# Kernel tuning notes

Measured on AMD Instinct MI355X. Metric: run time of the kernel, lower is better.

Reference implementation:

```python
import jax, jax.numpy as jnp
import numpy as np

TOPK = 2000        # post-score-sort candidates fed to NMS
NMS_THR = 0.5      # IOU suppression threshold


def get_iou(boxes1, boxes2):
    # boxes1: (A,4), boxes2: (B,4) in x1,y1,x2,y2 -> (A,B) IOU matrix
    area1 = (boxes1[:, 2] - boxes1[:, 0]) * (boxes1[:, 3] - boxes1[:, 1])
    area2 = (boxes2[:, 2] - boxes2[:, 0]) * (boxes2[:, 3] - boxes2[:, 1])
    lt = jnp.maximum(boxes1[:, None, :2], boxes2[None, :, :2])
    rb = jnp.minimum(boxes1[:, None, 2:], boxes2[None, :, 2:])
    wh = jnp.clip(rb - lt, 0.0)
    inter = wh[..., 0] * wh[..., 1]
    return inter / (area1[:, None] + area2[None, :] - inter)


def decode_boxes(box_transform_pred, boxes):
    # box_transform_pred: (N,C,4) dx,dy,dw,dh ; boxes: (N,4) -> (N,C,4)
    w = boxes[:, 2] - boxes[:, 0]
    h = boxes[:, 3] - boxes[:, 1]
    cx = boxes[:, 0] + 0.5 * w
    cy = boxes[:, 1] + 0.5 * h
    dx, dy, dw, dh = (box_transform_pred[..., i] for i in range(4))
    pcx = dx * w[:, None] + cx[:, None]
    pcy = dy * h[:, None] + cy[:, None]
    pw = jnp.exp(dw) * w[:, None]
    ph = jnp.exp(dh) * h[:, None]
    return jnp.stack((pcx - 0.5 * pw, pcy - 0.5 * ph,
                      pcx + 0.5 * pw, pcy + 0.5 * ph), axis=2)


def encode_boxes(gt, boxes):
    # boxes_to_transformation_targets: (N,4),(N,4) -> (N,4) tx,ty,tw,th
    w = boxes[:, 2] - boxes[:, 0]
    h = boxes[:, 3] - boxes[:, 1]
    cx = boxes[:, 0] + 0.5 * w
    cy = boxes[:, 1] + 0.5 * h
    gw = gt[:, 2] - gt[:, 0]
    gh = gt[:, 3] - gt[:, 1]
    gcx = gt[:, 0] + 0.5 * gw
    gcy = gt[:, 1] + 0.5 * gh
    return jnp.stack(((gcx - cx) / w, (gcy - cy) / h,
                      jnp.log(gw / w), jnp.log(gh / h)), axis=1)


def clamp_boxes(boxes, h, w):
    x1 = jnp.clip(boxes[..., 0], 0.0, w)
    y1 = jnp.clip(boxes[..., 1], 0.0, h)
    x2 = jnp.clip(boxes[..., 2], 0.0, w)
    y2 = jnp.clip(boxes[..., 3], 0.0, h)
    return jnp.stack((x1, y1, x2, y2), axis=-1)


def nms_keep(iou_kk, thr):
    # greedy NMS over score-sorted boxes; sequential via lax.scan
    K = iou_kk.shape[0]
    idx = jnp.arange(K)
    def step(suppressed, i):
        keep_i = ~suppressed[i]
        suppressed = suppressed | (keep_i & (iou_kk[i] > thr) & (idx > i))
        return suppressed, keep_i
    _, keep = jax.lax.scan(step, jnp.zeros((K,), bool), idx)
    return keep


def _make_boxes(key, n, h, w):
    k1, k2, k3, k4 = jax.random.split(key, 4)
    x1 = jax.random.uniform(k1, (n,)) * (w - 128.0)
    y1 = jax.random.uniform(k2, (n,)) * (h - 128.0)
    bw = jax.random.uniform(k3, (n,)) * 120.0 + 4.0
    bh = jax.random.uniform(k4, (n,)) * 120.0 + 4.0
    return jnp.stack((x1, y1, x1 + bw, y1 + bh), axis=1)


def setup_inputs() -> dict:
    key = jax.random.key(0)
    N, C, G, H, W = 200000, 21, 128, 800, 1333
    k1, k2, k3, k4 = jax.random.split(key, 4)
    return {
        "proposals": _make_boxes(k1, N, H, W),
        "box_transform_pred": jax.random.normal(k2, (N, C, 4)) * 0.1,
        "cls_scores": jax.random.normal(k3, (N, C)),
        "gt_boxes": _make_boxes(k4, G, H, W),
        "image_h": H,
        "image_w": W,
    }


def reference(proposals, box_transform_pred, cls_scores, gt_boxes, image_h, image_w):
    h = float(image_h); w = float(image_w)
    N = proposals.shape[0]
    # 1. decode all per-class boxes and clamp to image boundary  (N,C,4)
    pred_boxes = clamp_boxes(decode_boxes(box_transform_pred, proposals), h, w)
    iou = get_iou(gt_boxes, proposals)          # (G,N)
    best_idx = jnp.argmax(iou, axis=0)          # (N,)
    matched_gt = gt_boxes[best_idx]             # (N,4)
    reg_targets = encode_boxes(matched_gt, proposals)  # (N,4)
    # 3. per-proposal best foreground class score/box
    probs = jax.nn.softmax(cls_scores, axis=-1)
    fg = probs[:, 1:]
    score = jnp.max(fg, axis=-1)                # (N,)
    cls = jnp.argmax(fg, axis=-1) + 1           # (N,)
    idx = jnp.broadcast_to(cls[:, None, None], (N, 1, 4))
    box_per = jnp.take_along_axis(pred_boxes, idx, axis=1)[:, 0]  # (N,4)
    # 4. top-K by score, greedy NMS
    top_scores, top_idx = jax.lax.top_k(score, TOPK)
    top_boxes = box_per[top_idx]                # (K,4)
    keep = nms_keep(get_iou(top_boxes, top_boxes), NMS_THR)
    final = top_boxes * keep[:, None].astype(top_boxes.dtype)  # suppressed zeroed
    return jnp.concatenate([final, reg_targets], axis=0)
```

## Files before the change

kernel.cpp:

```cpp
#include <hip/hip_runtime.h>
#include <cstdint>

#define TOPK 2000
#define NMS_THR 0.5f
#define NCLS 21
#define HSHIFT 14
#define HBINS (1u << 16)
#define NCHUNK 256
#define CAND_CAP 4096
#define TPAD 2048

typedef unsigned long long u64;
typedef unsigned int u32;
typedef float f32x4 __attribute__((ext_vector_type(4)));

__device__ __forceinline__ u32 hperm(u32 bin) { return ((bin & 255u) << 8) | (bin >> 8); }

__device__ __forceinline__ float iou_pair(float ax1, float ay1, float ax2, float ay2, float aarea,
                                          float bx1, float by1, float bx2, float by2, float barea) {
#pragma clang fp contract(off)
    float ltx = fmaxf(ax1, bx1), lty = fmaxf(ay1, by1);
    float rbx = fminf(ax2, bx2), rby = fminf(ay2, by2);
    float wx = fmaxf(rbx - ltx, 0.f), wy = fmaxf(rby - lty, 0.f);
    float inter = wx * wy;
    return inter / (aarea + barea - inter);
}

__global__ __launch_bounds__(256) void k_prep(const float* __restrict__ cls,
                                              float* __restrict__ clsT,
                                              u32* __restrict__ hist, u32* __restrict__ csum,
                                              u32* __restrict__ meta, u32* __restrict__ rank,
                                              int N) {
    __shared__ float slds[256 * NCLS];
    int b = blockIdx.x, t = threadIdx.x;

    for (int v = b * 256 + t; v < (int)(HBINS / 4); v += gridDim.x * 256)
        ((uint4*)hist)[v] = make_uint4(0u, 0u, 0u, 0u);
    if (b == 0) {
        csum[t] = 0u;
        if (t < 64) meta[t] = 0u;
    }
    if (b < 16) rank[b * 256 + t] = 0u;

    int row0 = b * 256;
    int rows = N - row0;
    if (rows <= 0) return;
    if (rows > 256) rows = 256;
    if (rows == 256) {
        const uint4* __restrict__ src = (const uint4*)(cls + (size_t)row0 * NCLS);
        uint4* __restrict__ dst = (uint4*)slds;
        for (int v = t; v < 1344; v += 256) dst[v] = src[v];
    } else {
        int nw = rows * NCLS;
        const float* __restrict__ src = cls + (size_t)row0 * NCLS;
        for (int v = t; v < nw; v += 256) slds[v] = src[v];
    }
    __syncthreads();
    if (t < rows) {
#pragma unroll
        for (int c = 0; c < NCLS; ++c)
            clsT[(size_t)c * N + row0 + t] = slds[t * NCLS + c];
    }
}

__global__ __launch_bounds__(256, 3) void k_main(
    const float* __restrict__ prop, const float* __restrict__ btp,
    const float* __restrict__ clsT, const float* __restrict__ gt,
    const int* __restrict__ hptr, const int* __restrict__ wptr,
    float* __restrict__ out, float4* __restrict__ box_per,
    u32* __restrict__ score_bits, u32* __restrict__ hist,
    int N, int G) {
#pragma clang fp contract(off)
    __shared__ float4 sgt[256];
    __shared__ float sga[256];
    int tid = threadIdx.x;
    for (int g = tid; g < G; g += 256) {
        float4 gb = ((const float4*)gt)[g];
        sgt[g] = gb;
        sga[g] = (gb.z - gb.x) * (gb.w - gb.y);
    }
    __syncthreads();

    int i = blockIdx.x * 256 + tid;
    if (i >= N) return;

    float W = (float)wptr[0], H = (float)hptr[0];
    float4 p = ((const float4*)prop)[i];
    float pw = p.z - p.x, ph = p.w - p.y;
    float pcx = p.x + 0.5f * pw, pcy = p.y + 0.5f * ph;

    float e[NCLS];
#pragma unroll
    for (int c = 0; c < NCLS; ++c) e[c] = clsT[(size_t)c * N + i];

    float m = e[0];
#pragma unroll
    for (int c = 1; c < NCLS; ++c) m = fmaxf(m, e[c]);
#pragma unroll
    for (int c = 0; c < NCLS; ++c) e[c] = expf(e[c] - m);
    float Z = 0.f;
#pragma unroll
    for (int c = 0; c < NCLS; ++c) Z += e[c];
    float best = -1.f;
    int bc = 1;
#pragma unroll
    for (int c = 1; c < NCLS; ++c) {
        float pr = e[c] / Z;
        if (pr > best) { best = pr; bc = c; }
    }

    float4 t = ((const float4*)btp)[(size_t)i * NCLS + bc];

    u32 b = __float_as_uint(best);
    score_bits[i] = b;
    atomicAdd(&hist[hperm(b >> HSHIFT)], 1u);

    float parea = pw * ph;
    float bestiou = -1.f;
    int bi = 0;
    int g = 0;
    for (; g + 8 <= G; g += 8) {
        float4 g0 = sgt[g], g1 = sgt[g + 1], g2 = sgt[g + 2], g3 = sgt[g + 3];
        float4 g4 = sgt[g + 4], g5 = sgt[g + 5], g6 = sgt[g + 6], g7 = sgt[g + 7];
        float a0 = sga[g], a1 = sga[g + 1], a2 = sga[g + 2], a3 = sga[g + 3];
        float a4 = sga[g + 4], a5 = sga[g + 5], a6 = sga[g + 6], a7 = sga[g + 7];
        float v0 = iou_pair(g0.x, g0.y, g0.z, g0.w, a0, p.x, p.y, p.z, p.w, parea);
        float v1 = iou_pair(g1.x, g1.y, g1.z, g1.w, a1, p.x, p.y, p.z, p.w, parea);
        float v2 = iou_pair(g2.x, g2.y, g2.z, g2.w, a2, p.x, p.y, p.z, p.w, parea);
        float v3 = iou_pair(g3.x, g3.y, g3.z, g3.w, a3, p.x, p.y, p.z, p.w, parea);
        float v4 = iou_pair(g4.x, g4.y, g4.z, g4.w, a4, p.x, p.y, p.z, p.w, parea);
        float v5 = iou_pair(g5.x, g5.y, g5.z, g5.w, a5, p.x, p.y, p.z, p.w, parea);
        float v6 = iou_pair(g6.x, g6.y, g6.z, g6.w, a6, p.x, p.y, p.z, p.w, parea);
        float v7 = iou_pair(g7.x, g7.y, g7.z, g7.w, a7, p.x, p.y, p.z, p.w, parea);
        float va = v0; int ia = g;
        if (v1 > va) { va = v1; ia = g + 1; }
        float vb = v2; int ib = g + 2;
        if (v3 > vb) { vb = v3; ib = g + 3; }
        if (vb > va) { va = vb; ia = ib; }
        float vc = v4; int ic = g + 4;
        if (v5 > vc) { vc = v5; ic = g + 5; }
        float vd = v6; int id_ = g + 6;
        if (v7 > vd) { vd = v7; id_ = g + 7; }
        if (vd > vc) { vc = vd; ic = id_; }
        if (vc > va) { va = vc; ia = ic; }
        if (va > bestiou) { bestiou = va; bi = ia; }
    }
    for (; g < G; ++g) {
        float4 gb = sgt[g];
        float v = iou_pair(gb.x, gb.y, gb.z, gb.w, sga[g], p.x, p.y, p.z, p.w, parea);
        if (v > bestiou) { bestiou = v; bi = g; }
    }

    float qcx = t.x * pw + pcx, qcy = t.y * ph + pcy;
    float qw = expf(t.z) * pw, qh = expf(t.w) * ph;
    float bx1 = fminf(fmaxf(qcx - 0.5f * qw, 0.f), W);
    float by1 = fminf(fmaxf(qcy - 0.5f * qh, 0.f), H);
    float bx2 = fminf(fmaxf(qcx + 0.5f * qw, 0.f), W);
    float by2 = fminf(fmaxf(qcy + 0.5f * qh, 0.f), H);
    f32x4 bp = {bx1, by1, bx2, by2};
    __builtin_nontemporal_store(bp, (f32x4*)&box_per[i]);

    float4 mg = sgt[bi];
    float gw = mg.z - mg.x, gh = mg.w - mg.y;
    float gcx = mg.x + 0.5f * gw, gcy = mg.y + 0.5f * gh;
    f32x4 rt = {(gcx - pcx) / pw, (gcy - pcy) / ph, logf(gw / pw), logf(gh / ph)};
    __builtin_nontemporal_store(rt, (f32x4*)(out + 4 * (size_t)(TOPK + i)));
}

__global__ __launch_bounds__(256) void k_hsum_scan(const u32* __restrict__ hist,
                                                   u32* __restrict__ csum,
                                                   u32* __restrict__ meta) {
    __shared__ u32 ps[4];
    __shared__ u32 S[NCHUNK];
    __shared__ u32 sh_tc, sh_E;
    __shared__ int slast;
    int b = blockIdx.x, t = threadIdx.x;

    u32 v = hist[(size_t)t * 256 + b];
#pragma unroll
    for (int o = 32; o; o >>= 1) v += __shfl_xor(v, o);
    if ((t & 63) == 0) ps[t >> 6] = v;
    __syncthreads();
    if (t == 0) {
        u32 tot = ps[0] + ps[1] + ps[2] + ps[3];
        atomicAdd(&csum[b], tot);
        __threadfence();
        u32 old = atomicAdd(&meta[62], 1u);
        slast = (old == NCHUNK - 1u) ? 1 : 0;
    }
    __syncthreads();
    if (!slast) return;

    u32 c = atomicAdd(&csum[t], 0u);
    S[t] = c;
    __syncthreads();
    for (int off = 1; off < NCHUNK; off <<= 1) {
        u32 x = (t + off < NCHUNK) ? S[t + off] : 0u;
        __syncthreads();
        S[t] += x;
        __syncthreads();
    }
    u32 suff = S[t];
    u32 E = suff - c;
    if (suff >= TOPK && E < TOPK) { sh_tc = (u32)t; sh_E = E; }
    __syncthreads();
    u32 tc = sh_tc, E0 = sh_E;
    u32 hh = hist[(size_t)t * 256 + tc];
    __syncthreads();
    S[t] = hh;
    __syncthreads();
    for (int off = 1; off < NCHUNK; off <<= 1) {
        u32 x = (t + off < NCHUNK) ? S[t + off] : 0u;
        __syncthreads();
        S[t] += x;
        __syncthreads();
    }
    u32 tot2 = E0 + S[t];
    if (tot2 >= TOPK && (tot2 - hh) < TOPK) meta[0] = tc * 256u + (u32)t;
}

__global__ __launch_bounds__(256) void k_compact(const u32* __restrict__ score_bits,
                                                 const u32* __restrict__ meta, u32* __restrict__ cnt,
                                                 u64* __restrict__ keys, int N) {
    int i = blockIdx.x * 256 + threadIdx.x;
    if (i >= N) return;
    u32 b = score_bits[i];
    if ((b >> HSHIFT) >= meta[0]) {
        u32 pos = atomicAdd(cnt, 1u);
        if (pos < CAND_CAP) keys[pos] = ((u64)b << 32) | (u32)(~(u32)i);
    }
}

__global__ __launch_bounds__(256) void k_rank1(const u64* __restrict__ keys,
                                               const u32* __restrict__ meta,
                                               u32* __restrict__ rank) {
    __shared__ u64 sk[256];
    int it = blockIdx.x & 15, js = blockIdx.x >> 4;
    int t = threadIdx.x;
    u32 M = meta[1];
    if (M > CAND_CAP) M = CAND_CAP;
    u32 Mp = (M + 63u) & ~63u;
    u32 j0 = (u32)js * 256u;
    if (j0 >= Mp) return;
    u32 jn = Mp - j0; if (jn > 256u) jn = 256u;
    sk[t] = ((u32)t < jn && j0 + t < M) ? keys[j0 + t] : 0ull;
    __syncthreads();
    int idx = it * 256 + t;
    u64 k = (idx < (int)M) ? keys[idx] : ~0ull;
    u32 r = 0;
    int lane = t & 63;
    for (u32 jj = 0; jj < jn; jj += 64) {
        u64 tv = sk[jj + lane];
        u32 tlo = (u32)tv, thi = (u32)(tv >> 32);
#pragma unroll
        for (int l = 0; l < 64; ++l) {
            u64 kj = ((u64)(u32)__builtin_amdgcn_readlane(thi, l) << 32) |
                     (u64)(u32)__builtin_amdgcn_readlane(tlo, l);
            r += (kj > k) ? 1u : 0u;
        }
    }
    if (idx < (int)M && r) atomicAdd(&rank[idx], r);
}

__global__ __launch_bounds__(256) void k_rank2(const u64* __restrict__ keys,
                                               const u32* __restrict__ meta,
                                               const u32* __restrict__ rank,
                                               const float4* __restrict__ box_per,
                                               float4* __restrict__ topbox) {
    int idx = blockIdx.x * 256 + threadIdx.x;
    u32 M = meta[1];
    if (M > CAND_CAP) M = CAND_CAP;
    if (idx >= (int)M) return;
    u32 r = rank[idx];
    if (r < TOPK) {
        u64 k = keys[idx];
        topbox[r] = box_per[~(u32)(k & 0xffffffffull)];
    }
}

__global__ __launch_bounds__(256) void k_mask(const float4* __restrict__ topbox,
                                              u64* __restrict__ mask) {
#pragma clang fp contract(off)
    int gid = blockIdx.x * 256 + threadIdx.x;
    int w = gid >> 11, i = gid & (TPAD - 1);
    u64 m = 0;
    int j0 = w << 6;
    if (i < TOPK && j0 + 63 > i) {
        float4 a = topbox[i];
        float aarea = (a.z - a.x) * (a.w - a.y);
        for (int jj = 0; jj < 64; ++jj) {
            int j = j0 + jj;
            if (j < TOPK && j > i) {
                float4 b = topbox[j];
                float barea = (b.z - b.x) * (b.w - b.y);
                float v = iou_pair(a.x, a.y, a.z, a.w, aarea, b.x, b.y, b.z, b.w, barea);
                if (v > NMS_THR) m |= (1ull << jj);
            }
        }
    }
    mask[(size_t)i * 32 + w] = m;
}

__global__ __launch_bounds__(256) void k_nms(const u64* __restrict__ mask,
                                             const float4* __restrict__ topbox,
                                             float* __restrict__ out) {
    __shared__ u64 sm[2][64 * 32];
    __shared__ u64 srem[32];
    int t = threadIdx.x;
    int lane = t & 63;
    u32 lw = (u32)(lane & 31);
    u32 rlo = 0, rhi = 0;

    {
        const uint4* __restrict__ src = (const uint4*)mask;
        uint4 v0 = src[t], v1 = src[t + 256], v2 = src[t + 512], v3 = src[t + 768];
        uint4* __restrict__ dst = (uint4*)sm[0];
        dst[t] = v0; dst[t + 256] = v1; dst[t + 512] = v2; dst[t + 768] = v3;
    }
    __syncthreads();

    for (int c = 0; c < 32; ++c) {
        if (t >= 64 && t < 192) {
            if (c + 1 < 32) {
                const uint4* __restrict__ src = (const uint4*)(mask + (size_t)(c + 1) * 2048);
                uint4* __restrict__ dst = (uint4*)sm[(c + 1) & 1];
                int u = t - 64;
                uint4 v0 = src[u];
                uint4 v1 = src[u + 128];
                uint4 v2 = src[u + 256];
                uint4 v3 = src[u + 384];
                uint4 v4 = src[u + 512];
                uint4 v5 = src[u + 640];
                uint4 v6 = src[u + 768];
                uint4 v7 = src[u + 896];
                dst[u] = v0;
                dst[u + 128] = v1;
                dst[u + 256] = v2;
                dst[u + 384] = v3;
                dst[u + 512] = v4;
                dst[u + 640] = v5;
                dst[u + 768] = v6;
                dst[u + 896] = v7;
            }
        } else if (t < 64) {
            const u64* __restrict__ buf = sm[c & 1];
            u32 d_lo = (u32)__builtin_amdgcn_readlane(rlo, c);
            u32 d_hi = (u32)__builtin_amdgcn_readlane(rhi, c);
            u64 ring[8];
#pragma unroll
            for (int p = 0; p < 8; ++p) ring[p] = buf[p * 32 + lw];
#pragma unroll
            for (int l = 0; l < 64; ++l) {
                u64 row = ring[l & 7];
                if (l < 56) ring[l & 7] = buf[(l + 8) * 32 + lw];
                u32 r_lo = (u32)row, r_hi = (u32)(row >> 32);
                u32 sc_lo = (u32)__builtin_amdgcn_readlane(r_lo, c);
                u32 sc_hi = (u32)__builtin_amdgcn_readlane(r_hi, c);
                u32 bit = (l < 32) ? ((d_lo >> l) & 1u) : ((d_hi >> (l - 32)) & 1u);
                u32 mk = bit - 1u;
                d_lo |= sc_lo & mk;
                d_hi |= sc_hi & mk;
                rlo |= r_lo & mk;
                rhi |= r_hi & mk;
            }
        }
        __syncthreads();
    }
    if (t < 32) srem[t] = ((u64)rhi << 32) | rlo;
    __syncthreads();
    for (int r = t; r < TOPK; r += 256) {
        bool sup = (srem[r >> 6] >> (r & 63)) & 1ull;
        float4 b = topbox[r];
        ((float4*)out)[r] = sup ? make_float4(0.f, 0.f, 0.f, 0.f) : b;
    }
}

extern "C" void kernel_launch(void* const* d_in, const int* in_sizes, int n_in,
                              void* d_out, int out_size, void* d_ws, size_t ws_size,
                              hipStream_t stream) {
    const float* prop = (const float*)d_in[0];
    const float* btp = (const float*)d_in[1];
    const float* cls = (const float*)d_in[2];
    const float* gt = (const float*)d_in[3];
    const int* hptr = (const int*)d_in[4];
    const int* wptr = (const int*)d_in[5];
    float* out = (float*)d_out;
    int N = in_sizes[0] / 4;
    int G = in_sizes[3] / 4;
    if (G > 256) G = 256;

    char* ws = (char*)d_ws;
    size_t o = 0;
    u32* hist = (u32*)(ws + o);       o += (size_t)HBINS * 4;
    u32* csum = (u32*)(ws + o);       o += NCHUNK * 4;
    u32* meta = (u32*)(ws + o);       o += 256;
    u32* rank = (u32*)(ws + o);       o += (size_t)CAND_CAP * 4;
    u32* score_bits = (u32*)(ws + o); o += (((size_t)N * 4 + 255) & ~(size_t)255);
    u64* keys = (u64*)(ws + o);       o += (size_t)CAND_CAP * 8;
    float4* box_per = (float4*)(ws + o); o += (size_t)N * 16;
    float4* topbox = (float4*)(ws + o);  o += (size_t)TPAD * 16;
    u64* mask = (u64*)(ws + o);       o += (size_t)TPAD * 32 * 8;
    float* clsT = (float*)(ws + o);   o += (size_t)N * NCLS * 4;
    (void)o; (void)ws_size; (void)n_in; (void)out_size;

    int nb = (N + 255) / 256;
    k_prep<<<nb, 256, 0, stream>>>(cls, clsT, hist, csum, meta, rank, N);
    k_main<<<nb, 256, 0, stream>>>(prop, btp, clsT, gt, hptr, wptr, out, box_per, score_bits,
                                   hist, N, G);
    k_hsum_scan<<<NCHUNK, 256, 0, stream>>>(hist, csum, meta);
    k_compact<<<nb, 256, 0, stream>>>(score_bits, meta, meta + 1, keys, N);
    k_rank1<<<256, 256, 0, stream>>>(keys, meta, rank);
    k_rank2<<<CAND_CAP / 256, 256, 0, stream>>>(keys, meta, rank, box_per, topbox);
    k_mask<<<(32 * TPAD) / 256, 256, 0, stream>>>(topbox, mask);
    k_nms<<<1, 256, 0, stream>>>(mask, topbox, out);
}
```

Baseline: 261.9 us.

## Split NMS chunk step into diagonal-only serial pass and parallel row OR

k_mask now also writes each box's diagonal-block mask word to a separate diag array. The sequential NMS loop in k_nms resolves suppression within a 64-box chunk using only per-lane diagonal words held in registers through readlane, so the 64-step dependent chain no longer waits on LDS loads. The OR of kept rows into the remove mask is then done as a separate 32-iteration pass, with each half-wave covering 32 rows, and the two halves are combined by a shuffle at the end. This shortens the serial critical path of the single-block NMS. The cost is an extra global diag buffer and load per chunk.

```diff
diff --git a/kernel.cpp b/kernel.cpp
--- a/kernel.cpp
+++ b/kernel.cpp
@@ -279,7 +279,8 @@
 }
 
 __global__ __launch_bounds__(256) void k_mask(const float4* __restrict__ topbox,
-                                              u64* __restrict__ mask) {
+                                              u64* __restrict__ mask,
+                                              u64* __restrict__ diag) {
 #pragma clang fp contract(off)
     int gid = blockIdx.x * 256 + threadIdx.x;
     int w = gid >> 11, i = gid & (TPAD - 1);
@@ -299,15 +300,18 @@
         }
     }
     mask[(size_t)i * 32 + w] = m;
+    if (w == (i >> 6)) diag[i] = m;
 }
 
 __global__ __launch_bounds__(256) void k_nms(const u64* __restrict__ mask,
+                                             const u64* __restrict__ diag,
                                              const float4* __restrict__ topbox,
                                              float* __restrict__ out) {
     __shared__ u64 sm[2][64 * 32];
     __shared__ u64 srem[32];
     int t = threadIdx.x;
     int lane = t & 63;
+    int half = (lane >> 5) & 1;
     u32 lw = (u32)(lane & 31);
     u32 rlo = 0, rhi = 0;
 
@@ -317,6 +321,8 @@
         uint4* __restrict__ dst = (uint4*)sm[0];
         dst[t] = v0; dst[t + 256] = v1; dst[t + 512] = v2; dst[t + 768] = v3;
     }
+    u64 dg_cur = 0, dg_nxt = 0;
+    if (t < 64) dg_cur = diag[lane];
     __syncthreads();
 
     for (int c = 0; c < 32; ++c) {
@@ -343,30 +349,42 @@
                 dst[u + 896] = v7;
             }
         } else if (t < 64) {
+            if (c + 1 < 32) dg_nxt = diag[(c + 1) * 64 + lane];
             const u64* __restrict__ buf = sm[c & 1];
-            u32 d_lo = (u32)__builtin_amdgcn_readlane(rlo, c);
-            u32 d_hi = (u32)__builtin_amdgcn_readlane(rhi, c);
-            u64 ring[8];
-#pragma unroll
-            for (int p = 0; p < 8; ++p) ring[p] = buf[p * 32 + lw];
+
+            u32 dgl = (u32)dg_cur, dgh = (u32)(dg_cur >> 32);
+            u32 d_lo = (u32)__builtin_amdgcn_readlane(rlo, c) |
+                       (u32)__builtin_amdgcn_readlane(rlo, c + 32);
+            u32 d_hi = (u32)__builtin_amdgcn_readlane(rhi, c) |
+                       (u32)__builtin_amdgcn_readlane(rhi, c + 32);
 #pragma unroll
             for (int l = 0; l < 64; ++l) {
-                u64 row = ring[l & 7];
-                if (l < 56) ring[l & 7] = buf[(l + 8) * 32 + lw];
-                u32 r_lo = (u32)row, r_hi = (u32)(row >> 32);
-                u32 sc_lo = (u32)__builtin_amdgcn_readlane(r_lo, c);
-                u32 sc_hi = (u32)__builtin_amdgcn_readlane(r_hi, c);
+                u32 sc_lo = (u32)__builtin_amdgcn_readlane(dgl, l);
+                u32 sc_hi = (u32)__builtin_amdgcn_readlane(dgh, l);
                 u32 bit = (l < 32) ? ((d_lo >> l) & 1u) : ((d_hi >> (l - 32)) & 1u);
                 u32 mk = bit - 1u;
                 d_lo |= sc_lo & mk;
                 d_hi |= sc_hi & mk;
-                rlo |= r_lo & mk;
-                rhi |= r_hi & mk;
             }
+
+            u32 kept = half ? ~d_hi : ~d_lo;
+            int rbase = half << 5;
+#pragma unroll
+            for (int k = 0; k < 32; ++k) {
+                u64 row = buf[(rbase + k) * 32 + lw];
+                u32 mk = 0u - ((kept >> k) & 1u);
+                rlo |= (u32)row & mk;
+                rhi |= (u32)(row >> 32) & mk;
+            }
+            dg_cur = dg_nxt;
         }
         __syncthreads();
     }
-    if (t < 32) srem[t] = ((u64)rhi << 32) | rlo;
+    if (t < 64) {
+        u32 flo = rlo | (u32)__shfl_xor((int)rlo, 32);
+        u32 fhi = rhi | (u32)__shfl_xor((int)rhi, 32);
+        if (t < 32) srem[t] = ((u64)fhi << 32) | flo;
+    }
     __syncthreads();
     for (int r = t; r < TOPK; r += 256) {
         bool sup = (srem[r >> 6] >> (r & 63)) & 1ull;
@@ -400,6 +418,7 @@
     float4* box_per = (float4*)(ws + o); o += (size_t)N * 16;
     float4* topbox = (float4*)(ws + o);  o += (size_t)TPAD * 16;
     u64* mask = (u64*)(ws + o);       o += (size_t)TPAD * 32 * 8;
+    u64* diag = (u64*)(ws + o);       o += (size_t)TPAD * 8;
     float* clsT = (float*)(ws + o);   o += (size_t)N * NCLS * 4;
     (void)o; (void)ws_size; (void)n_in; (void)out_size;
 
@@ -411,6 +430,6 @@
     k_compact<<<nb, 256, 0, stream>>>(score_bits, meta, meta + 1, keys, N);
     k_rank1<<<256, 256, 0, stream>>>(keys, meta, rank);
     k_rank2<<<CAND_CAP / 256, 256, 0, stream>>>(keys, meta, rank, box_per, topbox);
-    k_mask<<<(32 * TPAD) / 256, 256, 0, stream>>>(topbox, mask);
-    k_nms<<<1, 256, 0, stream>>>(mask, topbox, out);
-}
+    k_mask<<<(32 * TPAD) / 256, 256, 0, stream>>>(topbox, mask, diag);
+    k_nms<<<1, 256, 0, stream>>>(mask, diag, topbox, out);
+}
```

Result: slower. 277.6 us (+6.0%).
